# Optimization experiments

Hardware: AMD Instinct MI355X
Metric: run time of the kernel (lower is better)

## Reference

```python
import jax, jax.numpy as jnp
import numpy as np

DIM = 3          # algebra dimension (3D Clifford algebra Cl(3,0))
NB = 2 ** DIM    # 8 blades
C_IN, C_OUT = 4, 4
K = 3            # conv kernel size
S = 48           # spatial size (== mask_size)
B = 4            # batch size
HID = 128


def _build_algebra():
    """Cayley table of Cl(3,0) with blades ordered by (grade, bitmask), and the
    path matrix M[p, bj, bk] = sum_bi cayley[bi,bj,bk] restricted to grade-triple p."""
    n = NB
    blades = sorted(range(n), key=lambda b: (bin(b).count('1'), b))
    idx = {b: i for i, b in enumerate(blades)}
    grades = np.array([bin(b).count('1') for b in blades])
    cay = np.zeros((n, n, n), dtype=np.float32)
    for a in range(n):
        for b in range(n):
            s = 1
            t = a >> 1
            while t:
                s *= (-1) ** bin(t & b).count('1')
                t >>= 1
            cay[idx[a], idx[b], idx[a ^ b]] = s  # Euclidean metric: no extra signs
    ng = DIM + 1
    path_id = -np.ones((ng, ng, ng), dtype=int)
    p = 0
    for gi in range(ng):
        for gj in range(ng):
            for gk in range(ng):
                if np.any(cay[np.ix_(np.where(grades == gi)[0], np.where(grades == gj)[0], np.where(grades == gk)[0])] != 0):
                    path_id[gi, gj, gk] = p
                    p += 1
    P = p  # == product_paths_sum == 20 for Cl(3,0)
    M = np.zeros((P, n, n), dtype=np.float32)
    for i in range(n):
        for j in range(n):
            for k in range(n):
                c = cay[i, j, k]
                if c != 0.0:
                    M[path_id[grades[i], grades[j], grades[k]], j, k] += c
    return M, P

CAYLEY_M, P = _build_algebra()


def _circular_mask(ks):
    c = (ks - 1) / 2.0
    zz, yy, xx = np.ogrid[:ks, :ks, :ks]
    d = np.sqrt((xx - c) ** 2 + (yy - c) ** 2 + (zz - c) ** 2)
    return (d <= c).astype(np.float32)


def _rel_pos_mv():
    """Kernel-grid offsets embedded as grade-1 multivectors: (K^3, NB)."""
    ax = np.linspace(-1.0, 1.0, K).astype(np.float32)
    gx, gy, gz = np.meshgrid(ax, ax, ax, indexing='ij')
    pos = np.stack([gx, gy, gz], -1).reshape(-1, DIM)
    mv = np.zeros((K ** DIM, NB), dtype=np.float32)
    mv[:, 1:1 + DIM] = pos  # grade-1 blade slots are indices 1..3
    return mv


def setup_inputs() -> dict:
    key = jax.random.key(0)
    ks = jax.random.split(key, 4)
    x = jax.random.normal(ks[0], (B, C_IN, S, S, S, NB), jnp.float32)
    w0 = jax.random.normal(ks[1], (2 * NB, HID), jnp.float32) / np.sqrt(2 * NB)
    w1 = jax.random.normal(ks[2], (HID, HID), jnp.float32) / np.sqrt(HID)
    w2 = jax.random.normal(ks[3], (HID, C_OUT * C_IN * P), jnp.float32) / np.sqrt(HID)
    return {
        'x': x,
        'w0': w0, 'b0': jnp.zeros((HID,), jnp.float32),
        'w1': w1, 'b1': jnp.zeros((HID,), jnp.float32),
        'w2': w2, 'b2': jnp.zeros((C_OUT * C_IN * P,), jnp.float32),
        'bias_param': jnp.zeros((C_OUT, 1, 1, 1, 1), jnp.float32),
    }


def reference(x, w0, b0, w1, b1, w2, b2, bias_param):
    # 1) masked global pooling -> per-sample per-blade condition (B, NB)
    mask = jnp.asarray(_circular_mask(S))
    cond = jnp.einsum('bcxyzn,xyz->bn', x, mask) / (mask.sum() * C_IN)

    # 2) per-sample dynamic kernel generation (vmapped kernel network)
    rel = jnp.asarray(_rel_pos_mv())               # (X, NB), X = K^3
    X = K ** DIM
    feat = jnp.concatenate([
        jnp.broadcast_to(rel[None], (B, X, NB)),
        jnp.broadcast_to(cond[:, None, :], (B, X, NB)),
    ], axis=-1)                                     # (B, X, 2*NB)
    h = jax.nn.gelu(feat @ w0 + b0)
    h = jax.nn.gelu(h @ w1 + b1)
    w = (h @ w2 + b2).reshape(B, X, C_OUT, C_IN, P)  # per-path geometric-product weights

    # 3) assemble blade-level kernel via sparse Cayley contraction
    M = jnp.asarray(CAYLEY_M)                       # (P, NB_in_blade, NB_out_blade)
    ker = jnp.einsum('bxoip,pjk->bokijx', w, M)     # (B, o, bk, i, bj, X)
    kernels = ker.reshape(B * C_OUT * NB, C_IN * NB, K, K, K)

    # 4) grouped conv: one kernel bank per sample (feature_group_count = B)
    inp = jnp.transpose(x, (0, 1, 5, 2, 3, 4)).reshape(1, B * C_IN * NB, S, S, S)
    out = jax.lax.conv_general_dilated(
        inp, kernels, window_strides=(1, 1, 1), padding='SAME',
        dimension_numbers=('NCDHW', 'OIDHW', 'NCDHW'), feature_group_count=B)
    out = out.reshape(B, C_OUT, NB, S, S, S)
    out = jnp.transpose(out, (0, 1, 3, 4, 5, 2))    # (B, c_out, S,S,S, NB)

    # 5) multivector bias embedded at blade dims (0,)
    bias = jnp.zeros((C_OUT, 1, 1, 1, NB), x.dtype).at[..., 0:1].set(bias_param)
    return out + bias
```

## Files before the change

### kernel.cpp

```cpp
#include <hip/hip_runtime.h>
#include <cmath>

#define SS 48
#define S3 110592
#define NB 8
#define CIN 4
#define COUT 4
#define HID 128
#define XT 27
#define NP 20
#define BATCH 4
#define PD 50
#define PD2 2500
#define PD3 125000
#define SLABV 648
#define SLABS 5184

typedef __attribute__((ext_vector_type(8))) short short8;
typedef __attribute__((ext_vector_type(4))) float f32x4;

struct Tables {
    int   pid[64];
    float sgn[64];
};

__device__ __forceinline__ unsigned short bf16_rne(float f) {
    union { float f; unsigned u; } c; c.f = f;
    unsigned r = c.u + 0x7FFF + ((c.u >> 16) & 1);
    return (unsigned short)(r >> 16);
}

__device__ __forceinline__ float gelu_tanh(float v) {
    const float c = 0.7978845608028654f;
    float u = c * (v + 0.044715f * v * v * v);
    return 0.5f * v * (1.0f + tanhf(u));
}

__global__ __launch_bounds__(256)
void pack_cond_kernel(const float* __restrict__ x, unsigned short* __restrict__ xb,
                      float* __restrict__ partial) {
    int b  = blockIdx.y;
    int pv = blockIdx.x * 256 + threadIdx.x;
    __shared__ float sacc[8];
    if (threadIdx.x < 8) sacc[threadIdx.x] = 0.0f;
    __syncthreads();
    float acc[8];
#pragma unroll
    for (int n = 0; n < 8; ++n) acc[n] = 0.0f;
    if (pv < PD3) {
        int zp = pv / PD2, rem = pv % PD2, yp = rem / PD, xp = rem % PD;
        int z = zp - 1, y = yp - 1, xx = xp - 1;
        unsigned short ob[32];
        bool interior = (unsigned)z < 48u && (unsigned)y < 48u && (unsigned)xx < 48u;
        if (interior) {
            int v = (z * 48 + y) * 48 + xx;
            float vals[32];
#pragma unroll
            for (int i = 0; i < 4; ++i) {
                const f32x4* p = (const f32x4*)(x + (((size_t)(b * 4 + i)) * S3 + v) * 8);
                f32x4 a = p[0], c4 = p[1];
                vals[i * 8 + 0] = a[0];  vals[i * 8 + 1] = a[1];
                vals[i * 8 + 2] = a[2];  vals[i * 8 + 3] = a[3];
                vals[i * 8 + 4] = c4[0]; vals[i * 8 + 5] = c4[1];
                vals[i * 8 + 6] = c4[2]; vals[i * 8 + 7] = c4[3];
            }
            int dx = 2 * xx - 47, dy = 2 * y - 47, dz = 2 * z - 47;
            if (dx * dx + dy * dy + dz * dz <= 2209) {
#pragma unroll
                for (int n = 0; n < 8; ++n)
                    acc[n] = vals[n] + vals[8 + n] + vals[16 + n] + vals[24 + n];
            }
#pragma unroll
            for (int k = 0; k < 32; ++k) ob[k] = bf16_rne(vals[k]);
        } else {
#pragma unroll
            for (int k = 0; k < 32; ++k) ob[k] = 0;
        }
        short8* dst = (short8*)(xb + ((size_t)b * PD3 + pv) * 32);
#pragma unroll
        for (int q = 0; q < 4; ++q) {
            short8 s;
#pragma unroll
            for (int e = 0; e < 8; ++e) s[e] = (short)ob[q * 8 + e];
            dst[q] = s;
        }
    }
#pragma unroll
    for (int n = 0; n < 8; ++n) {
        float a = acc[n];
        for (int off = 32; off; off >>= 1) a += __shfl_down(a, off);
        if ((threadIdx.x & 63) == 0) atomicAdd(&sacc[n], a);
    }
    __syncthreads();
    if (threadIdx.x < 8)
        partial[((size_t)b * 512 + blockIdx.x) * 8 + threadIdx.x] = sacc[threadIdx.x];
}

__global__ __launch_bounds__(320)
void mlp_fused(const float* __restrict__ partial,
               const float* __restrict__ w0, const float* __restrict__ b0,
               const float* __restrict__ w1, const float* __restrict__ b1,
               const float* __restrict__ w2, const float* __restrict__ b2,
               unsigned short* __restrict__ wb, float inv_norm, Tables tb) {
    int bx = blockIdx.x;
    int b = bx / XT, tap = bx % XT;
    int t = threadIdx.x;
    __shared__ float red[40][8];
    __shared__ float feat[16];
    __shared__ float h1[HID];
    __shared__ float h2[HID];
    __shared__ float wrow[320];
    {
        int ch = t & 7, seg = t >> 3;
        float s = 0.0f;
        for (int j = seg; j < 489; j += 40)
            s += partial[((size_t)b * 512 + j) * 8 + ch];
        red[seg][ch] = s;
    }
    __syncthreads();
    if (t < 8) {
        float s2 = 0.0f;
#pragma unroll
        for (int q = 0; q < 40; ++q) s2 += red[q][t];
        feat[8 + t] = s2 * inv_norm;
        float v = 0.0f;
        if (t == 1) v = (float)(tap / 9) - 1.0f;
        else if (t == 2) v = (float)((tap / 3) % 3) - 1.0f;
        else if (t == 3) v = (float)(tap % 3) - 1.0f;
        feat[t] = v;
    }
    __syncthreads();
    if (t < 128) {
        float s = b0[t];
#pragma unroll
        for (int k = 0; k < 16; ++k) s += feat[k] * w0[k * HID + t];
        h1[t] = gelu_tanh(s);
    }
    __syncthreads();
    if (t < 128) {
        float a0 = b1[t], a1 = 0.0f, a2 = 0.0f, a3 = 0.0f;
#pragma unroll
        for (int k = 0; k < HID; k += 4) {
            a0 += h1[k + 0] * w1[(k + 0) * HID + t];
            a1 += h1[k + 1] * w1[(k + 1) * HID + t];
            a2 += h1[k + 2] * w1[(k + 2) * HID + t];
            a3 += h1[k + 3] * w1[(k + 3) * HID + t];
        }
        h2[t] = gelu_tanh((a0 + a1) + (a2 + a3));
    }
    __syncthreads();
    {
        float a0 = b2[t], a1 = 0.0f, a2 = 0.0f, a3 = 0.0f;
#pragma unroll
        for (int k = 0; k < HID; k += 4) {
            a0 += h2[k + 0] * w2[(size_t)(k + 0) * 320 + t];
            a1 += h2[k + 1] * w2[(size_t)(k + 1) * 320 + t];
            a2 += h2[k + 2] * w2[(size_t)(k + 2) * 320 + t];
            a3 += h2[k + 3] * w2[(size_t)(k + 3) * 320 + t];
        }
        wrow[t] = (a0 + a1) + (a2 + a3);
    }
    __syncthreads();
    if (t < 128) {
        int m = t >> 2, cq = t & 3;
        int o = m >> 3, bk = m & 7;
        short8 sv;
#pragma unroll
        for (int e = 0; e < 8; ++e) {
            int c = cq * 8 + e;
            int i = c >> 3, bj = c & 7, jk = bj * 8 + bk;
            sv[e] = (short)bf16_rne(tb.sgn[jk] * wrow[o * 80 + i * 20 + tb.pid[jk]]);
        }
        int g  = (tap / 9) * 3 + (tap % 3);
        int ky = (tap % 9) / 3;
        int half = m >> 4, mm = m & 15;
        size_t tile = (size_t)(b * 27 + g * 3 + ky) * 1024;
        *(short8*)(wb + tile + half * 512 + (mm + cq * 16) * 8) = sv;
    }
}

__global__ __launch_bounds__(256, 3)
void conv_lds(const unsigned short* __restrict__ xb, const unsigned short* __restrict__ wb,
              const float* __restrict__ bias, float* __restrict__ out) {
    __shared__ __align__(16) short lds[4 * SLABS];
    int b  = blockIdx.y;
    int bx = blockIdx.x;
    int tx = bx % 3, ty = (bx / 3) % 12, tz = bx / 36;
    int X0 = tx * 16, Y0 = ty * 4, Z0 = tz * 4;
    int tid = threadIdx.x, lane = tid & 63, wave = tid >> 6;

    const unsigned short* xsrc = xb + (size_t)b * PD3 * 32 +
        ((size_t)Z0 * PD2 + (size_t)Y0 * PD + X0) * 32 + wave * 8;
#pragma unroll
    for (int k = 0; k < 11; ++k) {
        int h0 = k * 64, h = h0 + lane;
        if (h < SLABV) {
            int hz = h / 108, rem = h % 108, hy = rem / 18, hx = rem % 18;
            __builtin_amdgcn_global_load_lds(
                (const unsigned int*)(xsrc + ((size_t)hz * PD2 + hy * PD + hx) * 32),
                (unsigned int*)&lds[wave * SLABS + h0 * 8], 16, 0, 0);
        }
    }

    int col = lane & 15, kl = lane >> 4;
    const unsigned short* wgl = wb + (size_t)b * 27648 + lane * 8;
    __syncthreads();

    f32x4 acc[2][4];
#pragma unroll
    for (int mh = 0; mh < 2; ++mh)
#pragma unroll
        for (int r = 0; r < 4; ++r)
#pragma unroll
            for (int e = 0; e < 4; ++e) acc[mh][r][e] = 0.0f;

#pragma unroll
    for (int kz = 0; kz < 3; ++kz) {
        short8 wr0[9], wr1[9];
#pragma unroll
        for (int t9 = 0; t9 < 9; ++t9) {
            const unsigned short* p0 = wgl + (size_t)(kz * 9 + t9) * 1024;
            asm volatile("global_load_dwordx4 %0, %1, off" : "=v"(wr0[t9]) : "v"(p0));
            const unsigned short* p1 = p0 + 512;
            asm volatile("global_load_dwordx4 %0, %1, off" : "=v"(wr1[t9]) : "v"(p1));
        }
        asm volatile("s_waitcnt vmcnt(0)" ::: "memory");
        __builtin_amdgcn_sched_barrier(0);
#pragma unroll
        for (int kx = 0; kx < 3; ++kx) {
            const short* lb = &lds[kl * SLABS + ((wave + kz) * 108 + col + kx) * 8];
            short8 bfv[6];
#pragma unroll
            for (int u = 0; u < 6; ++u)
                bfv[u] = *(const short8*)(lb + u * 144);
#pragma unroll
            for (int ky = 0; ky < 3; ++ky) {
#pragma unroll
                for (int r = 0; r < 4; ++r) {
                    acc[0][r] = __builtin_amdgcn_mfma_f32_16x16x32_bf16(wr0[kx * 3 + ky], bfv[r + ky], acc[0][r], 0, 0, 0);
                    acc[1][r] = __builtin_amdgcn_mfma_f32_16x16x32_bf16(wr1[kx * 3 + ky], bfv[r + ky], acc[1][r], 0, 0, 0);
                }
            }
        }
    }

    int xc = X0 + col;
    int z  = Z0 + wave;
#pragma unroll
    for (int mh = 0; mh < 2; ++mh) {
        int m0 = kl * 4 + mh * 16;
        int o = m0 >> 3, bk0 = m0 & 7;
        float bi = (bk0 == 0) ? bias[o] : 0.0f;
#pragma unroll
        for (int r = 0; r < 4; ++r) {
            int y = Y0 + r;
            int vox = (z * 48 + y) * 48 + xc;
            f32x4 v = acc[mh][r];
            v[0] += bi;
            *(f32x4*)(out + (((size_t)(b * 4 + o)) * S3 + vox) * 8 + bk0) = v;
        }
    }
}

static inline int pc_host(int v) { return __builtin_popcount(v); }

extern "C" void kernel_launch(void* const* d_in, const int* in_sizes, int n_in,
                              void* d_out, int out_size, void* d_ws, size_t ws_size,
                              hipStream_t stream) {
    const float* x    = (const float*)d_in[0];
    const float* w0   = (const float*)d_in[1];
    const float* b0   = (const float*)d_in[2];
    const float* w1   = (const float*)d_in[3];
    const float* b1   = (const float*)d_in[4];
    const float* w2   = (const float*)d_in[5];
    const float* b2   = (const float*)d_in[6];
    const float* bias = (const float*)d_in[7];
    float* out = (float*)d_out;

    float* ws      = (float*)d_ws;
    float* partial = ws;
    unsigned short* wbb = (unsigned short*)(ws + 30272);
    unsigned short* xb  = wbb + 110592;

    int cnt = 0;
    for (int z = 0; z < SS; ++z) {
        int dz = 2 * z - 47;
        for (int y = 0; y < SS; ++y) {
            int dy = 2 * y - 47;
            for (int xx = 0; xx < SS; ++xx) {
                int dx = 2 * xx - 47;
                if (dx * dx + dy * dy + dz * dz <= 2209) ++cnt;
            }
        }
    }
    float inv_norm = 1.0f / ((float)cnt * (float)CIN);

    int pidtab[4][4][4];
    {
        bool ex[4][4][4] = {};
        for (int A = 0; A < 8; ++A)
            for (int B = 0; B < 8; ++B)
                ex[pc_host(A)][pc_host(B)][pc_host(A ^ B)] = true;
        int p = 0;
        for (int gi = 0; gi < 4; ++gi)
            for (int gj = 0; gj < 4; ++gj)
                for (int gk = 0; gk < 4; ++gk)
                    pidtab[gi][gj][gk] = ex[gi][gj][gk] ? p++ : -1;
    }
    static const int blades[8] = {0, 1, 2, 4, 3, 5, 6, 7};
    Tables tb;
    for (int bj = 0; bj < 8; ++bj) {
        for (int bk = 0; bk < 8; ++bk) {
            int bmj = blades[bj], bmk = blades[bk];
            int bma = bmj ^ bmk;
            int sgn = 1, t = bma >> 1;
            while (t) {
                if (pc_host(t & bmj) & 1) sgn = -sgn;
                t >>= 1;
            }
            tb.sgn[bj * 8 + bk] = (float)sgn;
            tb.pid[bj * 8 + bk] = pidtab[pc_host(bma)][pc_host(bmj)][pc_host(bmk)];
        }
    }

    pack_cond_kernel<<<dim3(489, BATCH), dim3(256), 0, stream>>>(x, xb, partial);
    mlp_fused<<<dim3(BATCH * XT), dim3(320), 0, stream>>>(partial, w0, b0, w1, b1, w2, b2,
                                                          wbb, inv_norm, tb);
    conv_lds<<<dim3(432, BATCH), dim3(256), 0, stream>>>(xb, wbb, bias, out);
}
```

Baseline: 65.56 us.

## Double-buffer per-kz weight loads in registers and stagger kz order across waves

Weight fragments for the next kz slice are now loaded into a second register set while MFMAs run on the current slice. Partial vmcnt waits replace the full drain before each slice. Each wave starts at a different kz, which spreads weight-load traffic, and MFMA sections raise wave priority with s_setprio. Holding two weight sets needs more VGPRs, so launch bounds drop from 3 to 2 blocks per SM, which lowers occupancy.

After: 66.25 us. Within noise of the previous version (+1.0%).

```diff
diff --git a/kernel.cpp b/kernel.cpp
--- a/kernel.cpp
+++ b/kernel.cpp
@@ -179,7 +179,7 @@
     }
 }
 
-__global__ __launch_bounds__(256, 3)
+__global__ __launch_bounds__(256, 2)
 void conv_lds(const unsigned short* __restrict__ xb, const unsigned short* __restrict__ wb,
               const float* __restrict__ bias, float* __restrict__ out) {
     __shared__ __align__(16) short lds[4 * SLABS];
@@ -204,7 +204,10 @@
 
     int col = lane & 15, kl = lane >> 4;
     const unsigned short* wgl = wb + (size_t)b * 27648 + lane * 8;
-    __syncthreads();
+
+    int kzA = wave % 3;
+    int kzB = (kzA + 1 >= 3) ? kzA - 2 : kzA + 1;
+    int kzC = (kzB + 1 >= 3) ? kzB - 2 : kzB + 1;
 
     f32x4 acc[2][4];
 #pragma unroll
@@ -214,18 +217,17 @@
 #pragma unroll
             for (int e = 0; e < 4; ++e) acc[mh][r][e] = 0.0f;
 
-#pragma unroll
-    for (int kz = 0; kz < 3; ++kz) {
-        short8 wr0[9], wr1[9];
+    short8 wa0[9], wa1[9], wb0[9], wb1[9];
+
+    auto issueW = [&](int kz, short8 (&w0)[9], short8 (&w1)[9]) {
 #pragma unroll
         for (int t9 = 0; t9 < 9; ++t9) {
-            const unsigned short* p0 = wgl + (size_t)(kz * 9 + t9) * 1024;
-            asm volatile("global_load_dwordx4 %0, %1, off" : "=v"(wr0[t9]) : "v"(p0));
-            const unsigned short* p1 = p0 + 512;
-            asm volatile("global_load_dwordx4 %0, %1, off" : "=v"(wr1[t9]) : "v"(p1));
-        }
-        asm volatile("s_waitcnt vmcnt(0)" ::: "memory");
-        __builtin_amdgcn_sched_barrier(0);
+            const unsigned short* p = wgl + (size_t)(kz * 9 + t9) * 1024;
+            asm volatile("global_load_dwordx4 %0, %1, off" : "=v"(w0[t9]) : "v"(p));
+            asm volatile("global_load_dwordx4 %0, %1, off" : "=v"(w1[t9]) : "v"(p + 512));
+        }
+    };
+    auto compute = [&](int kz, short8 (&w0)[9], short8 (&w1)[9]) {
 #pragma unroll
         for (int kx = 0; kx < 3; ++kx) {
             const short* lb = &lds[kl * SLABS + ((wave + kz) * 108 + col + kx) * 8];
@@ -233,16 +235,33 @@
 #pragma unroll
             for (int u = 0; u < 6; ++u)
                 bfv[u] = *(const short8*)(lb + u * 144);
+            __builtin_amdgcn_s_setprio(1);
 #pragma unroll
             for (int ky = 0; ky < 3; ++ky) {
 #pragma unroll
                 for (int r = 0; r < 4; ++r) {
-                    acc[0][r] = __builtin_amdgcn_mfma_f32_16x16x32_bf16(wr0[kx * 3 + ky], bfv[r + ky], acc[0][r], 0, 0, 0);
-                    acc[1][r] = __builtin_amdgcn_mfma_f32_16x16x32_bf16(wr1[kx * 3 + ky], bfv[r + ky], acc[1][r], 0, 0, 0);
+                    acc[0][r] = __builtin_amdgcn_mfma_f32_16x16x32_bf16(w0[kx * 3 + ky], bfv[r + ky], acc[0][r], 0, 0, 0);
+                    acc[1][r] = __builtin_amdgcn_mfma_f32_16x16x32_bf16(w1[kx * 3 + ky], bfv[r + ky], acc[1][r], 0, 0, 0);
                 }
             }
-        }
-    }
+            __builtin_amdgcn_s_setprio(0);
+        }
+    };
+
+    issueW(kzA, wa0, wa1);
+    __syncthreads();
+
+    issueW(kzB, wb0, wb1);
+    compute(kzA, wa0, wa1);
+
+    issueW(kzC, wa0, wa1);
+    asm volatile("s_waitcnt vmcnt(18)" ::: "memory");
+    __builtin_amdgcn_sched_barrier(0);
+    compute(kzB, wb0, wb1);
+
+    asm volatile("s_waitcnt vmcnt(0)" ::: "memory");
+    __builtin_amdgcn_sched_barrier(0);
+    compute(kzC, wa0, wa1);
 
     int xc = X0 + col;
     int z  = Z0 + wave;
```
